# Kernel optimization log

Measured on AMD Instinct MI355X. Metric: run time of the kernel, lower is better.

The kernel has to match this reference:

```python
import jax, jax.numpy as jnp
import numpy as np

# Config (matches init_kwargs)
D_MODEL = 1024
D_MLP = 4096
N_EXPERTS = 8
TOP_K = 2  # experts_per_token
BATCH = 1
POS = 2048


def setup_inputs() -> dict:
    key = jax.random.key(0)
    k0, k1, k2, k3, k4 = jax.random.split(key, 5)
    s = 0.02  # typical init scale
    x = jax.random.normal(k0, (BATCH, POS, D_MODEL), jnp.float32)
    W_gate = jax.random.normal(k1, (D_MODEL, N_EXPERTS), jnp.float32) * s  # router
    We_gate = jax.random.normal(k2, (N_EXPERTS, D_MODEL, D_MLP), jnp.float32) * s
    We_in = jax.random.normal(k3, (N_EXPERTS, D_MODEL, D_MLP), jnp.float32) * s
    We_out = jax.random.normal(k4, (N_EXPERTS, D_MLP, D_MODEL), jnp.float32) * s
    return {"x": x, "W_gate": W_gate, "We_gate": We_gate, "We_in": We_in, "We_out": We_out}


def reference(x, W_gate, We_gate, We_in, We_out):
    B, P, D = x.shape
    T = B * P
    E = W_gate.shape[1]
    h = x.reshape(T, D)  # [T, D]

    # Router: logits -> fp32 softmax -> top-k -> renormalize (as in torch code)
    logits = h @ W_gate  # [T, E]
    probs = jax.nn.softmax(logits.astype(jnp.float32), axis=-1)
    topw, topi = jax.lax.top_k(probs, TOP_K)  # [T, K]
    topw = topw / jnp.sum(topw, axis=-1, keepdims=True)
    topw = topw.astype(x.dtype)

    # Per-token combine weight for each expert (0 if not routed). [T, E]
    w_full = jnp.zeros((T, E), x.dtype).at[jnp.arange(T)[:, None], topi].add(topw)

    # Gated-MLP per expert; scan over the small fixed expert axis to avoid
    # materializing [E, T, D_MLP] hidden states at once.
    def per_expert(acc, params):
        Wg, Wi, Wo, we = params  # Wg/Wi: [D, D_MLP], Wo: [D_MLP, D], we: [T]
        hid = jax.nn.silu(h @ Wg) * (h @ Wi)  # [T, D_MLP]
        return acc + (hid @ Wo) * we[:, None], None

    res, _ = jax.lax.scan(
        per_expert,
        jnp.zeros((T, D), x.dtype),
        (We_gate, We_in, We_out, w_full.T),
    )
    return res.reshape(B, P, D)
```

## Files before the change

### kernel.cpp

```cpp
#include <hip/hip_runtime.h>
#include <hip/hip_bf16.h>

#define T_TOK 2048
#define DMODEL 1024
#define DMLP 4096
#define NEXP 8

typedef __bf16 bf16x8 __attribute__((ext_vector_type(8)));
typedef float f32x4 __attribute__((ext_vector_type(4)));

__device__ __forceinline__ unsigned short f2bf(float f) {
  return __builtin_bit_cast(unsigned short, (__bf16)f);
}

__global__ __launch_bounds__(64) void router_k(
    const float* __restrict__ x, const float* __restrict__ wg,
    int* __restrict__ topi, float* __restrict__ topw) {
  int t = blockIdx.x;
  int lane = threadIdx.x;
  const float* hx = x + (size_t)t * DMODEL;
  float acc[NEXP];
#pragma unroll
  for (int e = 0; e < NEXP; ++e) acc[e] = 0.f;
  for (int i = lane; i < DMODEL; i += 64) {
    float xi = hx[i];
    const float* w = wg + (size_t)i * NEXP;
#pragma unroll
    for (int e = 0; e < NEXP; ++e) acc[e] += xi * w[e];
  }
#pragma unroll
  for (int off = 32; off > 0; off >>= 1) {
#pragma unroll
    for (int e = 0; e < NEXP; ++e) acc[e] += __shfl_down(acc[e], off);
  }
  if (lane == 0) {
    float m = acc[0];
#pragma unroll
    for (int e = 1; e < NEXP; ++e) m = fmaxf(m, acc[e]);
    float p[NEXP], s = 0.f;
#pragma unroll
    for (int e = 0; e < NEXP; ++e) { p[e] = expf(acc[e] - m); s += p[e]; }
    float inv = 1.f / s;
#pragma unroll
    for (int e = 0; e < NEXP; ++e) p[e] *= inv;
    int i1 = 0;
#pragma unroll
    for (int e = 1; e < NEXP; ++e) if (p[e] > p[i1]) i1 = e;
    int i2 = (i1 == 0) ? 1 : 0;
#pragma unroll
    for (int e = 0; e < NEXP; ++e) if (e != i1 && p[e] > p[i2]) i2 = e;
    float w1 = p[i1], w2 = p[i2];
    float rs = 1.f / (w1 + w2);
    topi[2 * t] = i1;
    topi[2 * t + 1] = i2;
    topw[2 * t] = w1 * rs;
    topw[2 * t + 1] = w2 * rs;
  }
}

__global__ __launch_bounds__(512) void compact_k(
    const int* __restrict__ topi, const float* __restrict__ topw,
    int* __restrict__ offsets, int* __restrict__ perm,
    float* __restrict__ wrow) {
  int tid = threadIdx.x;
  int e = tid >> 6, lane = tid & 63;
  __shared__ int scnt[NEXP];
  __shared__ int soff[NEXP + 1];
  int c = 0;
  for (int j = lane; j < 2 * T_TOK; j += 64) {
    unsigned long long m = __ballot(topi[j] == e);
    c += __popcll(m);
  }
  if (lane == 0) scnt[e] = c;
  __syncthreads();
  if (tid == 0) {
    int s = 0;
    for (int k = 0; k < NEXP; ++k) { soff[k] = s; s += scnt[k]; }
    soff[NEXP] = s;
    for (int k = 0; k <= NEXP; ++k) offsets[k] = soff[k];
  }
  __syncthreads();
  int base = soff[e];
  for (int j = lane; j < 2 * T_TOK; j += 64) {
    bool f = (topi[j] == e);
    unsigned long long m = __ballot(f);
    if (f) {
      int p = base + __popcll(m & ((1ULL << lane) - 1ULL));
      perm[p] = j >> 1;
      wrow[p] = topw[j];
    }
    base += __popcll(m);
  }
}

#define BPITCH 40

__global__ __launch_bounds__(256) void hid_k(
    const float* __restrict__ x, const float* __restrict__ weg,
    const float* __restrict__ wei, const int* __restrict__ offsets,
    const int* __restrict__ perm, const float* __restrict__ wrow,
    unsigned short* __restrict__ hid) {
  int e = blockIdx.z;
  int off = offsets[e], end = offsets[e + 1];
  int cnt = end - off;
  int m0 = blockIdx.y * 128;
  if (m0 >= cnt) return;
  int nb = blockIdx.x * 64;
  const float* wg = weg + (size_t)e * DMODEL * DMLP;
  const float* wi = wei + (size_t)e * DMODEL * DMLP;

  __shared__ unsigned short As[128 * BPITCH];
  __shared__ unsigned short Bg[64 * BPITCH];
  __shared__ unsigned short Bi[64 * BPITCH];

  int tid = threadIdx.x;
  int lane = tid & 63, wid = tid >> 6;
  int wm = (wid & 1) * 64, wn = (wid >> 1) * 32;
  int lr = lane & 15, q = lane >> 4;

  f32x4 accg[4][2], acci[4][2];
  f32x4 z = {0.f, 0.f, 0.f, 0.f};
#pragma unroll
  for (int i = 0; i < 4; ++i)
#pragma unroll
    for (int j = 0; j < 2; ++j) { accg[i][j] = z; acci[i][j] = z; }

  const float* aptr[4];
  int adst[4];
#pragma unroll
  for (int it = 0; it < 4; ++it) {
    int task = tid + it * 256;
    int r = task >> 3, kc = (task & 7) * 4;
    int pl = m0 + r;
    int src = perm[off + ((pl < cnt) ? pl : 0)];
    aptr[it] = x + (size_t)src * DMODEL + kc;
    adst[it] = r * BPITCH + kc;
  }
  int tn = (tid & 15) * 4, tk = (tid >> 4) * 2;

  for (int k0 = 0; k0 < DMODEL; k0 += 32) {
#pragma unroll
    for (int it = 0; it < 4; ++it) {
      float4 v = *(const float4*)(aptr[it] + k0);
      ushort4 u;
      u.x = f2bf(v.x); u.y = f2bf(v.y); u.z = f2bf(v.z); u.w = f2bf(v.w);
      *(ushort4*)(&As[adst[it]]) = u;
    }
    {
      const float* pg = wg + (size_t)(k0 + tk) * DMLP + nb + tn;
      float4 g0 = *(const float4*)(pg);
      float4 g1 = *(const float4*)(pg + DMLP);
      const float* pi = wi + (size_t)(k0 + tk) * DMLP + nb + tn;
      float4 i0 = *(const float4*)(pi);
      float4 i1 = *(const float4*)(pi + DMLP);
      const float* c0 = (const float*)&g0;
      const float* c1 = (const float*)&g1;
      const float* d0 = (const float*)&i0;
      const float* d1 = (const float*)&i1;
#pragma unroll
      for (int cix = 0; cix < 4; ++cix) {
        ushort2 vg; vg.x = f2bf(c0[cix]); vg.y = f2bf(c1[cix]);
        *(ushort2*)(&Bg[(tn + cix) * BPITCH + tk]) = vg;
        ushort2 vi; vi.x = f2bf(d0[cix]); vi.y = f2bf(d1[cix]);
        *(ushort2*)(&Bi[(tn + cix) * BPITCH + tk]) = vi;
      }
    }
    __syncthreads();
    bf16x8 af[4], bgf[2], bif[2];
#pragma unroll
    for (int i = 0; i < 4; ++i)
      af[i] = *(const bf16x8*)(&As[(wm + i * 16 + lr) * BPITCH + q * 8]);
#pragma unroll
    for (int j = 0; j < 2; ++j) {
      bgf[j] = *(const bf16x8*)(&Bg[(wn + j * 16 + lr) * BPITCH + q * 8]);
      bif[j] = *(const bf16x8*)(&Bi[(wn + j * 16 + lr) * BPITCH + q * 8]);
    }
#pragma unroll
    for (int i = 0; i < 4; ++i)
#pragma unroll
      for (int j = 0; j < 2; ++j) {
        accg[i][j] = __builtin_amdgcn_mfma_f32_16x16x32_bf16(af[i], bgf[j], accg[i][j], 0, 0, 0);
        acci[i][j] = __builtin_amdgcn_mfma_f32_16x16x32_bf16(af[i], bif[j], acci[i][j], 0, 0, 0);
      }
    __syncthreads();
  }
#pragma unroll
  for (int i = 0; i < 4; ++i)
#pragma unroll
    for (int j = 0; j < 2; ++j)
#pragma unroll
      for (int r = 0; r < 4; ++r) {
        int row = wm + i * 16 + q * 4 + r;
        int pl = m0 + row;
        if (pl < cnt) {
          int pos = off + pl;
          float g = accg[i][j][r], vv = acci[i][j][r];
          float hv = (g / (1.f + expf(-g))) * vv * wrow[pos];
          hid[(size_t)pos * DMLP + nb + wn + j * 16 + lr] = f2bf(hv);
        }
      }
}

__global__ __launch_bounds__(256) void out_k(
    const unsigned short* __restrict__ hid, const float* __restrict__ weo,
    const int* __restrict__ offsets, const int* __restrict__ perm,
    float* __restrict__ out) {
  int e = blockIdx.z;
  int off = offsets[e], end = offsets[e + 1];
  int cnt = end - off;
  int m0 = blockIdx.y * 128;
  if (m0 >= cnt) return;
  int nb = blockIdx.x * 64;
  const float* wo = weo + (size_t)e * DMLP * DMODEL;

  __shared__ unsigned short As[128 * BPITCH];
  __shared__ unsigned short Bs[64 * BPITCH];

  int tid = threadIdx.x;
  int lane = tid & 63, wid = tid >> 6;
  int wm = (wid & 1) * 64, wn = (wid >> 1) * 32;
  int lr = lane & 15, q = lane >> 4;

  f32x4 acc[4][2];
  f32x4 z = {0.f, 0.f, 0.f, 0.f};
#pragma unroll
  for (int i = 0; i < 4; ++i)
#pragma unroll
    for (int j = 0; j < 2; ++j) acc[i][j] = z;

  const unsigned short* aptr[2];
  int adst[2];
#pragma unroll
  for (int it = 0; it < 2; ++it) {
    int task = tid + it * 256;
    int r = task >> 2, kg = (task & 3) * 8;
    int pl = m0 + r;
    int src = off + ((pl < cnt) ? pl : 0);
    aptr[it] = hid + (size_t)src * DMLP + kg;
    adst[it] = r * BPITCH + kg;
  }
  int tn = (tid & 15) * 4, tk = (tid >> 4) * 2;

  for (int k0 = 0; k0 < DMLP; k0 += 32) {
#pragma unroll
    for (int it = 0; it < 2; ++it) {
      uint4 v = *(const uint4*)(aptr[it] + k0);
      *(uint4*)(&As[adst[it]]) = v;
    }
    {
      const float* pb = wo + (size_t)(k0 + tk) * DMODEL + nb + tn;
      float4 b0 = *(const float4*)(pb);
      float4 b1 = *(const float4*)(pb + DMODEL);
      const float* c0 = (const float*)&b0;
      const float* c1 = (const float*)&b1;
#pragma unroll
      for (int cix = 0; cix < 4; ++cix) {
        ushort2 vb; vb.x = f2bf(c0[cix]); vb.y = f2bf(c1[cix]);
        *(ushort2*)(&Bs[(tn + cix) * BPITCH + tk]) = vb;
      }
    }
    __syncthreads();
    bf16x8 af[4], bf[2];
#pragma unroll
    for (int i = 0; i < 4; ++i)
      af[i] = *(const bf16x8*)(&As[(wm + i * 16 + lr) * BPITCH + q * 8]);
#pragma unroll
    for (int j = 0; j < 2; ++j)
      bf[j] = *(const bf16x8*)(&Bs[(wn + j * 16 + lr) * BPITCH + q * 8]);
#pragma unroll
    for (int i = 0; i < 4; ++i)
#pragma unroll
      for (int j = 0; j < 2; ++j)
        acc[i][j] = __builtin_amdgcn_mfma_f32_16x16x32_bf16(af[i], bf[j], acc[i][j], 0, 0, 0);
    __syncthreads();
  }
#pragma unroll
  for (int i = 0; i < 4; ++i)
#pragma unroll
    for (int j = 0; j < 2; ++j)
#pragma unroll
      for (int r = 0; r < 4; ++r) {
        int row = wm + i * 16 + q * 4 + r;
        int pl = m0 + row;
        if (pl < cnt) {
          int tok = perm[off + pl];
          atomicAdd(&out[(size_t)tok * DMODEL + nb + wn + j * 16 + lr],
                    acc[i][j][r]);
        }
      }
}

extern "C" void kernel_launch(void* const* d_in, const int* in_sizes, int n_in,
                              void* d_out, int out_size, void* d_ws,
                              size_t ws_size, hipStream_t stream) {
  const float* x = (const float*)d_in[0];
  const float* wgate = (const float*)d_in[1];
  const float* weg = (const float*)d_in[2];
  const float* wei = (const float*)d_in[3];
  const float* weo = (const float*)d_in[4];
  float* out = (float*)d_out;

  char* ws = (char*)d_ws;
  int* topi = (int*)(ws + 0);
  float* topw = (float*)(ws + (16 << 10));
  int* offsets = (int*)(ws + (32 << 10));
  int* perm = (int*)(ws + (33 << 10));
  float* wrow = (float*)(ws + (49 << 10));
  unsigned short* hid = (unsigned short*)(ws + (65 << 10));

  hipMemsetAsync(d_out, 0, (size_t)out_size * sizeof(float), stream);
  router_k<<<dim3(T_TOK), dim3(64), 0, stream>>>(x, wgate, topi, topw);
  compact_k<<<dim3(1), dim3(512), 0, stream>>>(topi, topw, offsets, perm, wrow);
  hid_k<<<dim3(DMLP / 64, T_TOK / 128, NEXP), dim3(256), 0, stream>>>(
      x, weg, wei, offsets, perm, wrow, hid);
  out_k<<<dim3(DMODEL / 64, T_TOK / 128, NEXP), dim3(256), 0, stream>>>(
      hid, weo, offsets, perm, out);
}
```

Before: 682.8 us.

## Use persistent M-loop grids, split-K out GEMM, coalesced B loads, parallel compaction

Result: slower. 720.8 us (+5.6%).

```diff
diff --git a/kernel.cpp b/kernel.cpp
--- a/kernel.cpp
+++ b/kernel.cpp
@@ -5,9 +5,11 @@
 #define DMODEL 1024
 #define DMLP 4096
 #define NEXP 8
+#define YB 4
 
 typedef __bf16 bf16x8 __attribute__((ext_vector_type(8)));
 typedef float f32x4 __attribute__((ext_vector_type(4)));
+typedef unsigned short u16x8 __attribute__((ext_vector_type(8)));
 
 __device__ __forceinline__ unsigned short f2bf(float f) {
   return __builtin_bit_cast(unsigned short, (__bf16)f);
@@ -63,33 +65,56 @@
     int* __restrict__ offsets, int* __restrict__ perm,
     float* __restrict__ wrow) {
   int tid = threadIdx.x;
-  int e = tid >> 6, lane = tid & 63;
-  __shared__ int scnt[NEXP];
-  __shared__ int soff[NEXP + 1];
-  int c = 0;
-  for (int j = lane; j < 2 * T_TOK; j += 64) {
-    unsigned long long m = __ballot(topi[j] == e);
-    c += __popcll(m);
-  }
-  if (lane == 0) scnt[e] = c;
+  int w = tid >> 6, lane = tid & 63;
+  __shared__ int hist[NEXP][NEXP];
+  __shared__ int base_s[NEXP][NEXP];
+  unsigned long long ltmask = (lane == 63) ? ~0ULL >> 1 : ((1ULL << lane) - 1ULL);
+
+  int c[NEXP];
+#pragma unroll
+  for (int ex = 0; ex < NEXP; ++ex) c[ex] = 0;
+  for (int it = 0; it < 8; ++it) {
+    int j = w * 512 + it * 64 + lane;
+    int e = topi[j];
+#pragma unroll
+    for (int ex = 0; ex < NEXP; ++ex) {
+      unsigned long long m = __ballot(e == ex);
+      c[ex] += __popcll(m);
+    }
+  }
+  if (lane == 0) {
+#pragma unroll
+    for (int ex = 0; ex < NEXP; ++ex) hist[w][ex] = c[ex];
+  }
   __syncthreads();
   if (tid == 0) {
     int s = 0;
-    for (int k = 0; k < NEXP; ++k) { soff[k] = s; s += scnt[k]; }
-    soff[NEXP] = s;
-    for (int k = 0; k <= NEXP; ++k) offsets[k] = soff[k];
+    for (int ex = 0; ex < NEXP; ++ex) {
+      offsets[ex] = s;
+      int t = s;
+      for (int w2 = 0; w2 < NEXP; ++w2) { base_s[w2][ex] = t; t += hist[w2][ex]; }
+      s = t;
+    }
+    offsets[NEXP] = s;
   }
   __syncthreads();
-  int base = soff[e];
-  for (int j = lane; j < 2 * T_TOK; j += 64) {
-    bool f = (topi[j] == e);
-    unsigned long long m = __ballot(f);
-    if (f) {
-      int p = base + __popcll(m & ((1ULL << lane) - 1ULL));
-      perm[p] = j >> 1;
-      wrow[p] = topw[j];
-    }
-    base += __popcll(m);
+  int rb[NEXP];
+#pragma unroll
+  for (int ex = 0; ex < NEXP; ++ex) rb[ex] = base_s[w][ex];
+  for (int it = 0; it < 8; ++it) {
+    int j = w * 512 + it * 64 + lane;
+    int e = topi[j];
+    float pw = topw[j];
+#pragma unroll
+    for (int ex = 0; ex < NEXP; ++ex) {
+      unsigned long long m = __ballot(e == ex);
+      if (e == ex) {
+        int p = rb[ex] + __popcll(m & ltmask);
+        perm[p] = j >> 1;
+        wrow[p] = pw;
+      }
+      rb[ex] += __popcll(m);
+    }
   }
 }
 
@@ -101,10 +126,7 @@
     const int* __restrict__ perm, const float* __restrict__ wrow,
     unsigned short* __restrict__ hid) {
   int e = blockIdx.z;
-  int off = offsets[e], end = offsets[e + 1];
-  int cnt = end - off;
-  int m0 = blockIdx.y * 128;
-  if (m0 >= cnt) return;
+  int off = offsets[e], cnt = offsets[e + 1] - off;
   int nb = blockIdx.x * 64;
   const float* wg = weg + (size_t)e * DMODEL * DMLP;
   const float* wi = wei + (size_t)e * DMODEL * DMLP;
@@ -118,87 +140,92 @@
   int wm = (wid & 1) * 64, wn = (wid >> 1) * 32;
   int lr = lane & 15, q = lane >> 4;
 
-  f32x4 accg[4][2], acci[4][2];
-  f32x4 z = {0.f, 0.f, 0.f, 0.f};
-#pragma unroll
-  for (int i = 0; i < 4; ++i)
-#pragma unroll
-    for (int j = 0; j < 2; ++j) { accg[i][j] = z; acci[i][j] = z; }
-
-  const float* aptr[4];
-  int adst[4];
-#pragma unroll
-  for (int it = 0; it < 4; ++it) {
-    int task = tid + it * 256;
-    int r = task >> 3, kc = (task & 7) * 4;
-    int pl = m0 + r;
-    int src = perm[off + ((pl < cnt) ? pl : 0)];
-    aptr[it] = x + (size_t)src * DMODEL + kc;
-    adst[it] = r * BPITCH + kc;
-  }
-  int tn = (tid & 15) * 4, tk = (tid >> 4) * 2;
-
-  for (int k0 = 0; k0 < DMODEL; k0 += 32) {
+  int bn = tid & 63, kq = tid >> 6;
+  const float* gsrc = wg + (size_t)(kq * 8) * DMLP + nb + bn;
+  const float* isrc = wi + (size_t)(kq * 8) * DMLP + nb + bn;
+  int bdst = bn * BPITCH + kq * 8;
+
+  for (int m0 = blockIdx.y * 128; m0 < cnt; m0 += YB * 128) {
+    const float* aptr[4];
+    int adst[4];
 #pragma unroll
     for (int it = 0; it < 4; ++it) {
-      float4 v = *(const float4*)(aptr[it] + k0);
-      ushort4 u;
-      u.x = f2bf(v.x); u.y = f2bf(v.y); u.z = f2bf(v.z); u.w = f2bf(v.w);
-      *(ushort4*)(&As[adst[it]]) = u;
-    }
-    {
-      const float* pg = wg + (size_t)(k0 + tk) * DMLP + nb + tn;
-      float4 g0 = *(const float4*)(pg);
-      float4 g1 = *(const float4*)(pg + DMLP);
-      const float* pi = wi + (size_t)(k0 + tk) * DMLP + nb + tn;
-      float4 i0 = *(const float4*)(pi);
-      float4 i1 = *(const float4*)(pi + DMLP);
-      const float* c0 = (const float*)&g0;
-      const float* c1 = (const float*)&g1;
-      const float* d0 = (const float*)&i0;
-      const float* d1 = (const float*)&i1;
-#pragma unroll
-      for (int cix = 0; cix < 4; ++cix) {
-        ushort2 vg; vg.x = f2bf(c0[cix]); vg.y = f2bf(c1[cix]);
-        *(ushort2*)(&Bg[(tn + cix) * BPITCH + tk]) = vg;
-        ushort2 vi; vi.x = f2bf(d0[cix]); vi.y = f2bf(d1[cix]);
-        *(ushort2*)(&Bi[(tn + cix) * BPITCH + tk]) = vi;
-      }
-    }
-    __syncthreads();
-    bf16x8 af[4], bgf[2], bif[2];
+      int task = tid + it * 256;
+      int r = task >> 3, kc = (task & 7) * 4;
+      int pl = m0 + r;
+      int src = perm[off + ((pl < cnt) ? pl : 0)];
+      aptr[it] = x + (size_t)src * DMODEL + kc;
+      adst[it] = r * BPITCH + kc;
+    }
+
+    f32x4 accg[4][2], acci[4][2];
+    f32x4 z = {0.f, 0.f, 0.f, 0.f};
 #pragma unroll
     for (int i = 0; i < 4; ++i)
-      af[i] = *(const bf16x8*)(&As[(wm + i * 16 + lr) * BPITCH + q * 8]);
-#pragma unroll
-    for (int j = 0; j < 2; ++j) {
-      bgf[j] = *(const bf16x8*)(&Bg[(wn + j * 16 + lr) * BPITCH + q * 8]);
-      bif[j] = *(const bf16x8*)(&Bi[(wn + j * 16 + lr) * BPITCH + q * 8]);
+#pragma unroll
+      for (int j = 0; j < 2; ++j) { accg[i][j] = z; acci[i][j] = z; }
+
+    for (int k0 = 0; k0 < DMODEL; k0 += 32) {
+#pragma unroll
+      for (int it = 0; it < 4; ++it) {
+        float4 v = *(const float4*)(aptr[it] + k0);
+        ushort4 u;
+        u.x = f2bf(v.x); u.y = f2bf(v.y); u.z = f2bf(v.z); u.w = f2bf(v.w);
+        *(ushort4*)(&As[adst[it]]) = u;
+      }
+      {
+        const float* pg = gsrc + (size_t)k0 * DMLP;
+        const float* pi = isrc + (size_t)k0 * DMLP;
+        float gv[8], iv[8];
+#pragma unroll
+        for (int kr = 0; kr < 8; ++kr) {
+          gv[kr] = pg[(size_t)kr * DMLP];
+          iv[kr] = pi[(size_t)kr * DMLP];
+        }
+        u16x8 ug, ui;
+#pragma unroll
+        for (int kr = 0; kr < 8; ++kr) {
+          ug[kr] = f2bf(gv[kr]);
+          ui[kr] = f2bf(iv[kr]);
+        }
+        *(u16x8*)(&Bg[bdst]) = ug;
+        *(u16x8*)(&Bi[bdst]) = ui;
+      }
+      __syncthreads();
+      bf16x8 af[4], bgf[2], bif[2];
+#pragma unroll
+      for (int i = 0; i < 4; ++i)
+        af[i] = *(const bf16x8*)(&As[(wm + i * 16 + lr) * BPITCH + q * 8]);
+#pragma unroll
+      for (int j = 0; j < 2; ++j) {
+        bgf[j] = *(const bf16x8*)(&Bg[(wn + j * 16 + lr) * BPITCH + q * 8]);
+        bif[j] = *(const bf16x8*)(&Bi[(wn + j * 16 + lr) * BPITCH + q * 8]);
+      }
+#pragma unroll
+      for (int i = 0; i < 4; ++i)
+#pragma unroll
+        for (int j = 0; j < 2; ++j) {
+          accg[i][j] = __builtin_amdgcn_mfma_f32_16x16x32_bf16(af[i], bgf[j], accg[i][j], 0, 0, 0);
+          acci[i][j] = __builtin_amdgcn_mfma_f32_16x16x32_bf16(af[i], bif[j], acci[i][j], 0, 0, 0);
+        }
+      __syncthreads();
     }
 #pragma unroll
     for (int i = 0; i < 4; ++i)
 #pragma unroll
-      for (int j = 0; j < 2; ++j) {
-        accg[i][j] = __builtin_amdgcn_mfma_f32_16x16x32_bf16(af[i], bgf[j], accg[i][j], 0, 0, 0);
-        acci[i][j] = __builtin_amdgcn_mfma_f32_16x16x32_bf16(af[i], bif[j], acci[i][j], 0, 0, 0);
-      }
-    __syncthreads();
-  }
-#pragma unroll
-  for (int i = 0; i < 4; ++i)
-#pragma unroll
-    for (int j = 0; j < 2; ++j)
-#pragma unroll
-      for (int r = 0; r < 4; ++r) {
-        int row = wm + i * 16 + q * 4 + r;
-        int pl = m0 + row;
-        if (pl < cnt) {
-          int pos = off + pl;
-          float g = accg[i][j][r], vv = acci[i][j][r];
-          float hv = (g / (1.f + expf(-g))) * vv * wrow[pos];
-          hid[(size_t)pos * DMLP + nb + wn + j * 16 + lr] = f2bf(hv);
-        }
-      }
+      for (int j = 0; j < 2; ++j)
+#pragma unroll
+        for (int r = 0; r < 4; ++r) {
+          int row = wm + i * 16 + q * 4 + r;
+          int pl = m0 + row;
+          if (pl < cnt) {
+            int pos = off + pl;
+            float g = accg[i][j][r], vv = acci[i][j][r];
+            float hv = (g / (1.f + expf(-g))) * vv * wrow[pos];
+            hid[(size_t)pos * DMLP + nb + wn + j * 16 + lr] = f2bf(hv);
+          }
+        }
+  }
 }
 
 __global__ __launch_bounds__(256) void out_k(
@@ -206,10 +233,9 @@
     const int* __restrict__ offsets, const int* __restrict__ perm,
     float* __restrict__ out) {
   int e = blockIdx.z;
-  int off = offsets[e], end = offsets[e + 1];
-  int cnt = end - off;
-  int m0 = blockIdx.y * 128;
-  if (m0 >= cnt) return;
+  int off = offsets[e], cnt = offsets[e + 1] - off;
+  int kh = blockIdx.y & 1;
+  int yb = blockIdx.y >> 1;
   int nb = blockIdx.x * 64;
   const float* wo = weo + (size_t)e * DMLP * DMODEL;
 
@@ -221,73 +247,76 @@
   int wm = (wid & 1) * 64, wn = (wid >> 1) * 32;
   int lr = lane & 15, q = lane >> 4;
 
-  f32x4 acc[4][2];
-  f32x4 z = {0.f, 0.f, 0.f, 0.f};
-#pragma unroll
-  for (int i = 0; i < 4; ++i)
-#pragma unroll
-    for (int j = 0; j < 2; ++j) acc[i][j] = z;
-
-  const unsigned short* aptr[2];
-  int adst[2];
-#pragma unroll
-  for (int it = 0; it < 2; ++it) {
-    int task = tid + it * 256;
-    int r = task >> 2, kg = (task & 3) * 8;
-    int pl = m0 + r;
-    int src = off + ((pl < cnt) ? pl : 0);
-    aptr[it] = hid + (size_t)src * DMLP + kg;
-    adst[it] = r * BPITCH + kg;
-  }
-  int tn = (tid & 15) * 4, tk = (tid >> 4) * 2;
-
-  for (int k0 = 0; k0 < DMLP; k0 += 32) {
+  int bn = tid & 63, kq = tid >> 6;
+  const float* bsrc = wo + (size_t)(kh * 2048 + kq * 8) * DMODEL + nb + bn;
+  int bdst = bn * BPITCH + kq * 8;
+
+  for (int m0 = yb * 128; m0 < cnt; m0 += YB * 128) {
+    const unsigned short* aptr[2];
+    int adst[2];
 #pragma unroll
     for (int it = 0; it < 2; ++it) {
-      uint4 v = *(const uint4*)(aptr[it] + k0);
-      *(uint4*)(&As[adst[it]]) = v;
-    }
-    {
-      const float* pb = wo + (size_t)(k0 + tk) * DMODEL + nb + tn;
-      float4 b0 = *(const float4*)(pb);
-      float4 b1 = *(const float4*)(pb + DMODEL);
-      const float* c0 = (const float*)&b0;
-      const float* c1 = (const float*)&b1;
-#pragma unroll
-      for (int cix = 0; cix < 4; ++cix) {
-        ushort2 vb; vb.x = f2bf(c0[cix]); vb.y = f2bf(c1[cix]);
-        *(ushort2*)(&Bs[(tn + cix) * BPITCH + tk]) = vb;
-      }
-    }
-    __syncthreads();
-    bf16x8 af[4], bf[2];
+      int task = tid + it * 256;
+      int r = task >> 2, kg = (task & 3) * 8;
+      int pl = m0 + r;
+      int src = off + ((pl < cnt) ? pl : 0);
+      aptr[it] = hid + (size_t)src * DMLP + kh * 2048 + kg;
+      adst[it] = r * BPITCH + kg;
+    }
+
+    f32x4 acc[4][2];
+    f32x4 z = {0.f, 0.f, 0.f, 0.f};
 #pragma unroll
     for (int i = 0; i < 4; ++i)
-      af[i] = *(const bf16x8*)(&As[(wm + i * 16 + lr) * BPITCH + q * 8]);
-#pragma unroll
-    for (int j = 0; j < 2; ++j)
-      bf[j] = *(const bf16x8*)(&Bs[(wn + j * 16 + lr) * BPITCH + q * 8]);
+#pragma unroll
+      for (int j = 0; j < 2; ++j) acc[i][j] = z;
+
+    for (int kk = 0; kk < 2048; kk += 32) {
+#pragma unroll
+      for (int it = 0; it < 2; ++it) {
+        uint4 v = *(const uint4*)(aptr[it] + kk);
+        *(uint4*)(&As[adst[it]]) = v;
+      }
+      {
+        const float* pb = bsrc + (size_t)kk * DMODEL;
+        float bv[8];
+#pragma unroll
+        for (int kr = 0; kr < 8; ++kr) bv[kr] = pb[(size_t)kr * DMODEL];
+        u16x8 ub;
+#pragma unroll
+        for (int kr = 0; kr < 8; ++kr) ub[kr] = f2bf(bv[kr]);
+        *(u16x8*)(&Bs[bdst]) = ub;
+      }
+      __syncthreads();
+      bf16x8 af[4], bfr[2];
+#pragma unroll
+      for (int i = 0; i < 4; ++i)
+        af[i] = *(const bf16x8*)(&As[(wm + i * 16 + lr) * BPITCH + q * 8]);
+#pragma unroll
+      for (int j = 0; j < 2; ++j)
+        bfr[j] = *(const bf16x8*)(&Bs[(wn + j * 16 + lr) * BPITCH + q * 8]);
+#pragma unroll
+      for (int i = 0; i < 4; ++i)
+#pragma unroll
+        for (int j = 0; j < 2; ++j)
+          acc[i][j] = __builtin_amdgcn_mfma_f32_16x16x32_bf16(af[i], bfr[j], acc[i][j], 0, 0, 0);
+      __syncthreads();
+    }
 #pragma unroll
     for (int i = 0; i < 4; ++i)
 #pragma unroll
       for (int j = 0; j < 2; ++j)
-        acc[i][j] = __builtin_amdgcn_mfma_f32_16x16x32_bf16(af[i], bf[j], acc[i][j], 0, 0, 0);
-    __syncthreads();
-  }
-#pragma unroll
-  for (int i = 0; i < 4; ++i)
-#pragma unroll
-    for (int j = 0; j < 2; ++j)
-#pragma unroll
-      for (int r = 0; r < 4; ++r) {
-        int row = wm + i * 16 + q * 4 + r;
-        int pl = m0 + row;
-        if (pl < cnt) {
-          int tok = perm[off + pl];
-          atomicAdd(&out[(size_t)tok * DMODEL + nb + wn + j * 16 + lr],
-                    acc[i][j][r]);
-        }
-      }
+#pragma unroll
+        for (int r = 0; r < 4; ++r) {
+          int row = wm + i * 16 + q * 4 + r;
+          int pl = m0 + row;
+          if (pl < cnt) {
+            int tok = perm[off + pl];
+            atomicAdd(&out[(size_t)tok * DMODEL + nb + wn + j * 16 + lr],
+                      acc[i][j][r]);
+          }
+        }
+  }
 }
 
 extern "C" void kernel_launch(void* const* d_in, const int* in_sizes, int n_in,
@@ -311,8 +340,8 @@
   hipMemsetAsync(d_out, 0, (size_t)out_size * sizeof(float), stream);
   router_k<<<dim3(T_TOK), dim3(64), 0, stream>>>(x, wgate, topi, topw);
   compact_k<<<dim3(1), dim3(512), 0, stream>>>(topi, topw, offsets, perm, wrow);
-  hid_k<<<dim3(DMLP / 64, T_TOK / 128, NEXP), dim3(256), 0, stream>>>(
+  hid_k<<<dim3(DMLP / 64, YB, NEXP), dim3(256), 0, stream>>>(
       x, weg, wei, offsets, perm, wrow, hid);
-  out_k<<<dim3(DMODEL / 64, T_TOK / 128, NEXP), dim3(256), 0, stream>>>(
+  out_k<<<dim3(DMODEL / 64, 2 * YB, NEXP), dim3(256), 0, stream>>>(
       hid, weo, offsets, perm, out);
 }
```
